# Kernel tuning notes

Measured on AMD Instinct MI355X. Metric: run time of the kernel, lower is better.

The kernel has to match this reference:

```python
import jax, jax.numpy as jnp
import numpy as np

C, H, W, NC, LC = 512, 160, 160, 1203, 64


def setup_inputs() -> dict:
    key = jax.random.key(0)
    ks = jax.random.split(key, 8)
    return {
        "cls_feat": jax.random.normal(ks[0], (1, C, H, W), jnp.float32),
        "loc_feat": jax.random.normal(ks[1], (1, LC, H, W), jnp.float32),
        "conf": jax.random.uniform(ks[2], (1,), jnp.float32, 0.2, 0.8),
        "pf_w": jax.random.normal(ks[3], (C,), jnp.float32) * 0.02,   # pf 1x1 conv, C->1
        "pf_b": jnp.zeros((1,), jnp.float32),
        "vocab_w": jax.random.normal(ks[4], (NC, C), jnp.float32) * 0.02,  # conv2linear weight
        "vocab_b": jnp.zeros((NC,), jnp.float32),
        "loc_w": jax.random.normal(ks[5], (LC, LC), jnp.float32) * 0.02,   # loc 1x1 conv
        "loc_b": jnp.zeros((LC,), jnp.float32),
    }


def reference(cls_feat, loc_feat, conf, pf_w, pf_b, vocab_w, vocab_b, loc_w, loc_b):
    B, Cc, Hh, Ww = cls_feat.shape
    # proposal-filter score: 1x1 conv C->1 on batch 0, flattened to [HW]
    pf_score = jnp.einsum('c,chw->hw', pf_w, cls_feat[0]).reshape(-1) + pf_b  # [HW]
    mask = jax.nn.sigmoid(pf_score) > conf[0]  # [HW] bool
    # tokens: [1, HW, C]
    tok = cls_feat.reshape(B, Cc, Hh * Ww).transpose(0, 2, 1)
    # static-shape equivalent of the proposal filter: zero masked-out tokens
    tok = tok * mask[None, :, None].astype(tok.dtype)
    # vocab linear (converted 1x1 conv): [1, HW, NC] -> [1, NC, HW]
    cls_out = (jnp.einsum('bnc,vc->bnv', tok, vocab_w) + vocab_b).transpose(0, 2, 1)
    # localization 1x1 conv
    loc_out = jnp.einsum('oi,bihw->bohw', loc_w, loc_feat) + loc_b[None, :, None, None]
    return loc_out, cls_out, mask
```

## Files before the change

### kernel.cpp

```cpp
#include <hip/hip_runtime.h>
#include <math.h>


constexpr int C_    = 512;
constexpr int HW_   = 25600;
constexpr int NC_   = 1203;
constexpr int VPAD_ = 1216;

constexpr int LOC_OFF_  = 0;
constexpr int CLS_OFF_  = 64 * HW_;
constexpr int MASK_OFF_ = CLS_OFF_ + NC_ * HW_;

constexpr int PF_BLOCKS_    = HW_ / 64;
constexpr int TRANS_BLOCKS_ = 19 * 8;
constexpr int GEMM_BLOCKS_  = 19 * 256;
constexpr int LOC_BLOCKS_   = 400;
constexpr int FILL_BLOCKS_  = 2048;

typedef float vfloat4 __attribute__((ext_vector_type(4)));

__global__ void k_init(int* cnt) { *cnt = 0; }

__global__ __launch_bounds__(256) void k_pre(
    const float* __restrict__ cls_feat, const float* __restrict__ conf,
    const float* __restrict__ pf_w, const float* __restrict__ pf_b,
    const float* __restrict__ vocab_w, float* __restrict__ out,
    int* __restrict__ cnt, int* __restrict__ idxList,
    float* __restrict__ AT4, int jcap)
{
    const int bid = blockIdx.x;
    const int tid = threadIdx.x;

    if (bid < PF_BLOCKS_) {
        __shared__ double sPart[256];
        const int hwi   = tid & 63;
        const int slice = tid >> 6;
        const int hw    = bid * 64 + hwi;
        const float* p  = cls_feat + (size_t)slice * 128 * HW_ + hw;
        const float* w  = pf_w + slice * 128;
        double acc = 0.0;
        #pragma unroll 4
        for (int k = 0; k < 128; ++k)
            acc += (double)w[k] * (double)p[(size_t)k * HW_];
        sPart[tid] = acc;
        __syncthreads();
        if (slice == 0) {
            double s = sPart[hwi] + sPart[64 + hwi] + sPart[128 + hwi] +
                       sPart[192 + hwi] + (double)pf_b[0];
            double sig = 1.0 / (1.0 + exp(-s));
            bool m = sig > (double)conf[0];
            out[MASK_OFF_ + hw] = m ? 1.0f : 0.0f;
            if (m) {
                int pos = atomicAdd(cnt, 1);
                if (pos < HW_) idxList[pos] = hw;
            }
        }
    } else {
        if (jcap <= 0) return;
        const int tb = bid - PF_BLOCKS_;
        const int v0 = (tb % 19) * 64;
        const int k0 = (tb / 19) * 64;
        __shared__ float t[64][65];
        const int c  = tid & 63;
        const int r4 = tid >> 6;
        #pragma unroll
        for (int i = 0; i < 16; ++i) {
            const int r = r4 * 16 + i;
            const int v = v0 + r;
            t[r][c] = (v < NC_) ? vocab_w[(size_t)v * C_ + k0 + c] : 0.f;
        }
        __syncthreads();
        #pragma unroll
        for (int i = 0; i < 16; ++i) {
            const int k  = r4 * 16 + i;
            const int kg = k0 + k;
            AT4[((size_t)(kg >> 2) * VPAD_ + v0 + c) * 4 + (kg & 3)] = t[c][k];
        }
    }
}

__global__ __launch_bounds__(256) void k_gatherJ(
    const float* __restrict__ cls_feat, const int* __restrict__ cnt,
    const int* __restrict__ idxList, float* __restrict__ BdT, int jcap)
{
    const int count = min(*cnt, HW_);
    if (count > jcap) return;
    const int t = threadIdx.x;
    for (int j = blockIdx.x; j < count; j += gridDim.x) {
        const int hw = idxList[j];
        BdT[(size_t)j * C_ + t]       = cls_feat[(size_t)t * HW_ + hw];
        BdT[(size_t)j * C_ + 256 + t] = cls_feat[(size_t)(256 + t) * HW_ + hw];
    }
}

__global__ __launch_bounds__(256) void k_mega(
    const float* __restrict__ loc_feat, const float* __restrict__ vocab_b,
    const float* __restrict__ loc_w, const float* __restrict__ loc_b,
    const float* __restrict__ AT4, const int* __restrict__ cnt,
    const float* __restrict__ BdT, float* __restrict__ clsTmp,
    float* __restrict__ out, int jcap)
{
    const int bid = blockIdx.x;
    const int tid = threadIdx.x;

    if (bid < GEMM_BLOCKS_) {
        const int count = min(*cnt, HW_);
        if (count == 0 || count > jcap) return;
        const int jBase = (bid / 19) * 4;
        if (jBase >= count) return;

        const int lane = tid & 63;
        const int w    = __builtin_amdgcn_readfirstlane(tid >> 6);
        const int v0   = (bid % 19) * 64;
        const int v    = v0 + lane;
        const float* __restrict__ Acol = AT4 + (size_t)v * 4;

        const int j0 = jBase + 0, j1 = jBase + 1, j2 = jBase + 2, j3 = jBase + 3;
        const float* __restrict__ B0 = BdT + (size_t)(j0 < count ? j0 : 0) * C_;
        const float* __restrict__ B1 = BdT + (size_t)(j1 < count ? j1 : 0) * C_;
        const float* __restrict__ B2 = BdT + (size_t)(j2 < count ? j2 : 0) * C_;
        const float* __restrict__ B3 = BdT + (size_t)(j3 < count ? j3 : 0) * C_;

        vfloat4 ac0 = {0,0,0,0}, ac1 = {0,0,0,0}, ac2 = {0,0,0,0}, ac3 = {0,0,0,0};
        const int kqBeg = w * 32;
        #pragma unroll 8
        for (int q = 0; q < 32; ++q) {
            const int kq = kqBeg + q;
            const vfloat4 a  = *(const vfloat4*)(Acol + (size_t)kq * VPAD_ * 4);
            const vfloat4 b0 = *(const vfloat4*)(B0 + kq * 4);
            const vfloat4 b1 = *(const vfloat4*)(B1 + kq * 4);
            const vfloat4 b2 = *(const vfloat4*)(B2 + kq * 4);
            const vfloat4 b3 = *(const vfloat4*)(B3 + kq * 4);
            ac0 += a * b0; ac1 += a * b1; ac2 += a * b2; ac3 += a * b3;
        }

        __shared__ float sRed[4][4][64];
        sRed[w][0][lane] = (ac0.x + ac0.y) + (ac0.z + ac0.w);
        sRed[w][1][lane] = (ac1.x + ac1.y) + (ac1.z + ac1.w);
        sRed[w][2][lane] = (ac2.x + ac2.y) + (ac2.z + ac2.w);
        sRed[w][3][lane] = (ac3.x + ac3.y) + (ac3.z + ac3.w);
        __syncthreads();

        if (tid < 64) {
            const float bias = (v < NC_) ? vocab_b[v] : 0.f;
            #pragma unroll
            for (int jj = 0; jj < 4; ++jj) {
                const int j = jBase + jj;
                if (j < count) {
                    const float s =
                        (sRed[0][jj][lane] + sRed[1][jj][lane]) +
                        (sRed[2][jj][lane] + sRed[3][jj][lane]);
                    clsTmp[(size_t)j * VPAD_ + v] = s + bias;
                }
            }
        }
    } else if (bid < GEMM_BLOCKS_ + LOC_BLOCKS_) {
        const int j   = bid - GEMM_BLOCKS_;
        const int hwb = j % 100;
        const int o0  = (j / 100) * 16;
        __shared__ float sw[16][64];
        for (int i = tid; i < 16 * 64; i += 256)
            sw[i >> 6][i & 63] = loc_w[(o0 + (i >> 6)) * 64 + (i & 63)];
        __syncthreads();
        const int hw = hwb * 256 + tid;
        float acc[16];
        #pragma unroll
        for (int r = 0; r < 16; ++r) acc[r] = loc_b[o0 + r];
        for (int i = 0; i < 64; ++i) {
            float f = loc_feat[(size_t)i * HW_ + hw];
            #pragma unroll
            for (int r = 0; r < 16; ++r) acc[r] += sw[r][i] * f;
        }
        #pragma unroll
        for (int r = 0; r < 16; ++r)
            out[LOC_OFF_ + (size_t)(o0 + r) * HW_ + hw] = acc[r];
    } else {
        const int fb = bid - GEMM_BLOCKS_ - LOC_BLOCKS_;
        const int total4 = NC_ * HW_ / 4;
        vfloat4* o = (vfloat4*)(out + CLS_OFF_);
        for (int i = fb * 256 + tid; i < total4; i += FILL_BLOCKS_ * 256) {
            int v = i / (HW_ / 4);
            float b = vocab_b[v];
            vfloat4 val = {b, b, b, b};
            __builtin_nontemporal_store(val, &o[i]);
        }
    }
}

__global__ __launch_bounds__(256) void k_scatter(
    const int* __restrict__ cnt, const int* __restrict__ idxList,
    const float* __restrict__ clsTmp, float* __restrict__ out, int jcap)
{
    const int count = min(*cnt, HW_);
    if (count > jcap) return;
    const int j = blockIdx.x;
    if (j >= count) return;
    const int hw = idxList[j];
    const float* __restrict__ src = clsTmp + (size_t)j * VPAD_;
    for (int v = threadIdx.x; v < NC_; v += 256)
        out[CLS_OFF_ + (size_t)v * HW_ + hw] = src[v];
}

__global__ __launch_bounds__(256) void k_gemm_fallback(
    const float* __restrict__ cls_feat, const float* __restrict__ vocab_w,
    const float* __restrict__ vocab_b, const int* __restrict__ cnt,
    const int* __restrict__ idxList, float* __restrict__ out, int capB)
{
    const int count = min(*cnt, HW_);
    if (count <= capB) return;
    const int v0 = blockIdx.x * 64;

    __shared__ float sAT[16][64];
    __shared__ float sBT[16][64];
    __shared__ int   sIdx[64];

    const int tid = threadIdx.x;
    const int tx = tid & 15;
    const int ty = tid >> 4;
    const int r  = tid >> 2;
    const int kq = tid & 3;

    for (int jb = blockIdx.y; (jb << 6) < count; jb += gridDim.y) {
        const int j0 = jb << 6;
        __syncthreads();
        if (tid < 64) {
            int j = j0 + tid;
            sIdx[tid] = (j < count) ? idxList[j] : -1;
        }
        __syncthreads();
        const int hwj = sIdx[r];

        float acc[4][4] = {};
        for (int k0 = 0; k0 < C_; k0 += 16) {
            float4 a4 = make_float4(0.f, 0.f, 0.f, 0.f);
            if (v0 + r < NC_)
                a4 = *(const float4*)(vocab_w + (size_t)(v0 + r) * C_ + k0 + kq * 4);
            float b0 = 0.f, b1 = 0.f, b2 = 0.f, b3 = 0.f;
            if (hwj >= 0) {
                const float* bp = cls_feat + (size_t)(k0 + kq * 4) * HW_ + hwj;
                b0 = bp[0]; b1 = bp[HW_]; b2 = bp[2 * HW_]; b3 = bp[3 * HW_];
            }
            __syncthreads();
            sAT[kq * 4 + 0][r] = a4.x; sAT[kq * 4 + 1][r] = a4.y;
            sAT[kq * 4 + 2][r] = a4.z; sAT[kq * 4 + 3][r] = a4.w;
            sBT[kq * 4 + 0][r] = b0;   sBT[kq * 4 + 1][r] = b1;
            sBT[kq * 4 + 2][r] = b2;   sBT[kq * 4 + 3][r] = b3;
            __syncthreads();
            #pragma unroll
            for (int kk = 0; kk < 16; ++kk) {
                const float4 av = *(const float4*)&sAT[kk][ty * 4];
                const float4 bv = *(const float4*)&sBT[kk][tx * 4];
                acc[0][0] += av.x * bv.x; acc[0][1] += av.x * bv.y;
                acc[0][2] += av.x * bv.z; acc[0][3] += av.x * bv.w;
                acc[1][0] += av.y * bv.x; acc[1][1] += av.y * bv.y;
                acc[1][2] += av.y * bv.z; acc[1][3] += av.y * bv.w;
                acc[2][0] += av.z * bv.x; acc[2][1] += av.z * bv.y;
                acc[2][2] += av.z * bv.z; acc[2][3] += av.z * bv.w;
                acc[3][0] += av.w * bv.x; acc[3][1] += av.w * bv.y;
                acc[3][2] += av.w * bv.z; acc[3][3] += av.w * bv.w;
            }
        }
        #pragma unroll
        for (int a = 0; a < 4; ++a) {
            int v = v0 + ty * 4 + a;
            if (v >= NC_) continue;
            float bias = vocab_b[v];
            #pragma unroll
            for (int b = 0; b < 4; ++b) {
                int j = j0 + tx * 4 + b;
                if (j < count) {
                    int hw = sIdx[tx * 4 + b];
                    out[CLS_OFF_ + (size_t)v * HW_ + hw] = acc[a][b] + bias;
                }
            }
        }
    }
}

extern "C" void kernel_launch(void* const* d_in, const int* in_sizes, int n_in,
                              void* d_out, int out_size, void* d_ws,
                              size_t ws_size, hipStream_t stream) {
    const float* cls_feat = (const float*)d_in[0];
    const float* loc_feat = (const float*)d_in[1];
    const float* conf     = (const float*)d_in[2];
    const float* pf_w     = (const float*)d_in[3];
    const float* pf_b     = (const float*)d_in[4];
    const float* vocab_w  = (const float*)d_in[5];
    const float* vocab_b  = (const float*)d_in[6];
    const float* loc_w    = (const float*)d_in[7];
    const float* loc_b    = (const float*)d_in[8];
    float* out = (float*)d_out;

    int*   cnt      = (int*)d_ws;
    int*   idxList  = (int*)((char*)d_ws + 4096);
    size_t fixed    = 4096 + (size_t)HW_ * sizeof(int);
    size_t atBytes  = (size_t)(C_ / 4) * VPAD_ * 4 * sizeof(float);
    size_t bdtBytes = (size_t)1024 * C_ * sizeof(float);
    size_t tmpBytes = (size_t)1024 * VPAD_ * sizeof(float);
    float* AT4      = (float*)((char*)d_ws + fixed);
    float* BdT      = (float*)((char*)d_ws + fixed + atBytes);
    float* clsTmp   = (float*)((char*)d_ws + fixed + atBytes + bdtBytes);

    int jcap = 0;
    if (ws_size >= fixed + atBytes + bdtBytes + tmpBytes) jcap = 1024;

    hipLaunchKernelGGL(k_init, dim3(1), dim3(1), 0, stream, cnt);
    hipLaunchKernelGGL(k_pre, dim3(PF_BLOCKS_ + TRANS_BLOCKS_), dim3(256),
                       0, stream,
                       cls_feat, conf, pf_w, pf_b, vocab_w, out, cnt,
                       idxList, AT4, jcap);
    if (jcap > 0) {
        hipLaunchKernelGGL(k_gatherJ, dim3(512), dim3(256), 0, stream,
                           cls_feat, cnt, idxList, BdT, jcap);
    }
    hipLaunchKernelGGL(k_mega,
                       dim3(GEMM_BLOCKS_ + LOC_BLOCKS_ + FILL_BLOCKS_),
                       dim3(256), 0, stream,
                       loc_feat, vocab_b, loc_w, loc_b, AT4, cnt, BdT,
                       clsTmp, out, jcap);
    if (jcap > 0) {
        hipLaunchKernelGGL(k_scatter, dim3(1024), dim3(256), 0, stream,
                           cnt, idxList, clsTmp, out, jcap);
    }
    hipLaunchKernelGGL(k_gemm_fallback, dim3((NC_ + 63) / 64, 8), dim3(256),
                       0, stream, cls_feat, vocab_w, vocab_b, cnt, idxList,
                       out, jcap);
}
```

Before: 68.71 us.

## Fuse cls scatter into bias fill via per-pixel row lookup table

The pre-pass now writes, for each pixel, its compacted row index, or -1 when the pixel is masked out. The bias-fill loop reads this table and writes GEMM results from clsTmp straight into the output, so the separate scatter kernel and its strided writes go away. The sparse GEMM moves out of the mega kernel into its own launch so its results are ready before the fill runs. This adds one launch, one lookup-table read per output vector and gathered reads from clsTmp, and the GEMM no longer overlaps with the loc/fill work.

```diff
diff --git a/kernel.cpp b/kernel.cpp
--- a/kernel.cpp
+++ b/kernel.cpp
@@ -13,7 +13,6 @@
 
 constexpr int PF_BLOCKS_    = HW_ / 64;
 constexpr int TRANS_BLOCKS_ = 19 * 8;
-constexpr int GEMM_BLOCKS_  = 19 * 256;
 constexpr int LOC_BLOCKS_   = 400;
 constexpr int FILL_BLOCKS_  = 2048;
 
@@ -26,7 +25,7 @@
     const float* __restrict__ pf_w, const float* __restrict__ pf_b,
     const float* __restrict__ vocab_w, float* __restrict__ out,
     int* __restrict__ cnt, int* __restrict__ idxList,
-    float* __restrict__ AT4, int jcap)
+    int* __restrict__ jLut, float* __restrict__ AT4, int jcap)
 {
     const int bid = blockIdx.x;
     const int tid = threadIdx.x;
@@ -50,10 +49,12 @@
             double sig = 1.0 / (1.0 + exp(-s));
             bool m = sig > (double)conf[0];
             out[MASK_OFF_ + hw] = m ? 1.0f : 0.0f;
+            int pos = -1;
             if (m) {
-                int pos = atomicAdd(cnt, 1);
+                pos = atomicAdd(cnt, 1);
                 if (pos < HW_) idxList[pos] = hw;
             }
+            jLut[hw] = (m && pos >= 0 && pos < jcap) ? pos : -1;
         }
     } else {
         if (jcap <= 0) return;
@@ -93,69 +94,75 @@
     }
 }
 
+__global__ __launch_bounds__(256) void k_gemm6t(
+    const float* __restrict__ AT4, const float* __restrict__ vocab_b,
+    const int* __restrict__ cnt, const float* __restrict__ BdT,
+    float* __restrict__ clsTmp, int jcap)
+{
+    const int count = min(*cnt, HW_);
+    if (count == 0 || count > jcap) return;
+    const int jBase = blockIdx.y * 4;
+    if (jBase >= count) return;
+
+    const int tid  = threadIdx.x;
+    const int lane = tid & 63;
+    const int w    = __builtin_amdgcn_readfirstlane(tid >> 6);
+    const int v0   = blockIdx.x * 64;
+    const int v    = v0 + lane;
+    const float* __restrict__ Acol = AT4 + (size_t)v * 4;
+
+    const int j0 = jBase + 0, j1 = jBase + 1, j2 = jBase + 2, j3 = jBase + 3;
+    const float* __restrict__ B0 = BdT + (size_t)(j0 < count ? j0 : 0) * C_;
+    const float* __restrict__ B1 = BdT + (size_t)(j1 < count ? j1 : 0) * C_;
+    const float* __restrict__ B2 = BdT + (size_t)(j2 < count ? j2 : 0) * C_;
+    const float* __restrict__ B3 = BdT + (size_t)(j3 < count ? j3 : 0) * C_;
+
+    vfloat4 ac0 = {0,0,0,0}, ac1 = {0,0,0,0}, ac2 = {0,0,0,0}, ac3 = {0,0,0,0};
+    const int kqBeg = w * 32;
+    #pragma unroll 8
+    for (int q = 0; q < 32; ++q) {
+        const int kq = kqBeg + q;
+        const vfloat4 a  = *(const vfloat4*)(Acol + (size_t)kq * VPAD_ * 4);
+        const vfloat4 b0 = *(const vfloat4*)(B0 + kq * 4);
+        const vfloat4 b1 = *(const vfloat4*)(B1 + kq * 4);
+        const vfloat4 b2 = *(const vfloat4*)(B2 + kq * 4);
+        const vfloat4 b3 = *(const vfloat4*)(B3 + kq * 4);
+        ac0 += a * b0; ac1 += a * b1; ac2 += a * b2; ac3 += a * b3;
+    }
+
+    __shared__ float sRed[4][4][64];
+    sRed[w][0][lane] = (ac0.x + ac0.y) + (ac0.z + ac0.w);
+    sRed[w][1][lane] = (ac1.x + ac1.y) + (ac1.z + ac1.w);
+    sRed[w][2][lane] = (ac2.x + ac2.y) + (ac2.z + ac2.w);
+    sRed[w][3][lane] = (ac3.x + ac3.y) + (ac3.z + ac3.w);
+    __syncthreads();
+
+    if (tid < 64) {
+        const float bias = (v < NC_) ? vocab_b[v] : 0.f;
+        #pragma unroll
+        for (int jj = 0; jj < 4; ++jj) {
+            const int j = jBase + jj;
+            if (j < count) {
+                const float s =
+                    (sRed[0][jj][lane] + sRed[1][jj][lane]) +
+                    (sRed[2][jj][lane] + sRed[3][jj][lane]);
+                clsTmp[(size_t)j * VPAD_ + v] = s + bias;
+            }
+        }
+    }
+}
+
 __global__ __launch_bounds__(256) void k_mega(
     const float* __restrict__ loc_feat, const float* __restrict__ vocab_b,
     const float* __restrict__ loc_w, const float* __restrict__ loc_b,
-    const float* __restrict__ AT4, const int* __restrict__ cnt,
-    const float* __restrict__ BdT, float* __restrict__ clsTmp,
-    float* __restrict__ out, int jcap)
+    const int* __restrict__ cnt, const int* __restrict__ jLut,
+    const float* __restrict__ clsTmp, float* __restrict__ out, int jcap)
 {
     const int bid = blockIdx.x;
     const int tid = threadIdx.x;
 
-    if (bid < GEMM_BLOCKS_) {
-        const int count = min(*cnt, HW_);
-        if (count == 0 || count > jcap) return;
-        const int jBase = (bid / 19) * 4;
-        if (jBase >= count) return;
-
-        const int lane = tid & 63;
-        const int w    = __builtin_amdgcn_readfirstlane(tid >> 6);
-        const int v0   = (bid % 19) * 64;
-        const int v    = v0 + lane;
-        const float* __restrict__ Acol = AT4 + (size_t)v * 4;
-
-        const int j0 = jBase + 0, j1 = jBase + 1, j2 = jBase + 2, j3 = jBase + 3;
-        const float* __restrict__ B0 = BdT + (size_t)(j0 < count ? j0 : 0) * C_;
-        const float* __restrict__ B1 = BdT + (size_t)(j1 < count ? j1 : 0) * C_;
-        const float* __restrict__ B2 = BdT + (size_t)(j2 < count ? j2 : 0) * C_;
-        const float* __restrict__ B3 = BdT + (size_t)(j3 < count ? j3 : 0) * C_;
-
-        vfloat4 ac0 = {0,0,0,0}, ac1 = {0,0,0,0}, ac2 = {0,0,0,0}, ac3 = {0,0,0,0};
-        const int kqBeg = w * 32;
-        #pragma unroll 8
-        for (int q = 0; q < 32; ++q) {
-            const int kq = kqBeg + q;
-            const vfloat4 a  = *(const vfloat4*)(Acol + (size_t)kq * VPAD_ * 4);
-            const vfloat4 b0 = *(const vfloat4*)(B0 + kq * 4);
-            const vfloat4 b1 = *(const vfloat4*)(B1 + kq * 4);
-            const vfloat4 b2 = *(const vfloat4*)(B2 + kq * 4);
-            const vfloat4 b3 = *(const vfloat4*)(B3 + kq * 4);
-            ac0 += a * b0; ac1 += a * b1; ac2 += a * b2; ac3 += a * b3;
-        }
-
-        __shared__ float sRed[4][4][64];
-        sRed[w][0][lane] = (ac0.x + ac0.y) + (ac0.z + ac0.w);
-        sRed[w][1][lane] = (ac1.x + ac1.y) + (ac1.z + ac1.w);
-        sRed[w][2][lane] = (ac2.x + ac2.y) + (ac2.z + ac2.w);
-        sRed[w][3][lane] = (ac3.x + ac3.y) + (ac3.z + ac3.w);
-        __syncthreads();
-
-        if (tid < 64) {
-            const float bias = (v < NC_) ? vocab_b[v] : 0.f;
-            #pragma unroll
-            for (int jj = 0; jj < 4; ++jj) {
-                const int j = jBase + jj;
-                if (j < count) {
-                    const float s =
-                        (sRed[0][jj][lane] + sRed[1][jj][lane]) +
-                        (sRed[2][jj][lane] + sRed[3][jj][lane]);
-                    clsTmp[(size_t)j * VPAD_ + v] = s + bias;
-                }
-            }
-        }
-    } else if (bid < GEMM_BLOCKS_ + LOC_BLOCKS_) {
-        const int j   = bid - GEMM_BLOCKS_;
+    if (bid < LOC_BLOCKS_) {
+        const int j   = bid;
         const int hwb = j % 100;
         const int o0  = (j / 100) * 16;
         __shared__ float sw[16][64];
@@ -175,30 +182,31 @@
         for (int r = 0; r < 16; ++r)
             out[LOC_OFF_ + (size_t)(o0 + r) * HW_ + hw] = acc[r];
     } else {
-        const int fb = bid - GEMM_BLOCKS_ - LOC_BLOCKS_;
+        const int fb     = bid - LOC_BLOCKS_;
+        const int count  = min(*cnt, HW_);
+        const bool live  = (jcap > 0) && (count > 0) && (count <= jcap);
+        const int hw4    = HW_ / 4;
         const int total4 = NC_ * HW_ / 4;
+        const int4* jLut4 = (const int4*)jLut;
         vfloat4* o = (vfloat4*)(out + CLS_OFF_);
         for (int i = fb * 256 + tid; i < total4; i += FILL_BLOCKS_ * 256) {
-            int v = i / (HW_ / 4);
-            float b = vocab_b[v];
+            const int v   = i / hw4;
+            const int rem = i - v * hw4;
+            const float b = vocab_b[v];
             vfloat4 val = {b, b, b, b};
+            if (live) {
+                const int4 jl = jLut4[rem];
+                if ((jl.x | jl.y | jl.z | jl.w) >= 0 ||
+                    jl.x >= 0 || jl.y >= 0 || jl.z >= 0 || jl.w >= 0) {
+                    if (jl.x >= 0) val.x = clsTmp[(size_t)jl.x * VPAD_ + v];
+                    if (jl.y >= 0) val.y = clsTmp[(size_t)jl.y * VPAD_ + v];
+                    if (jl.z >= 0) val.z = clsTmp[(size_t)jl.z * VPAD_ + v];
+                    if (jl.w >= 0) val.w = clsTmp[(size_t)jl.w * VPAD_ + v];
+                }
+            }
             __builtin_nontemporal_store(val, &o[i]);
         }
     }
-}
-
-__global__ __launch_bounds__(256) void k_scatter(
-    const int* __restrict__ cnt, const int* __restrict__ idxList,
-    const float* __restrict__ clsTmp, float* __restrict__ out, int jcap)
-{
-    const int count = min(*cnt, HW_);
-    if (count > jcap) return;
-    const int j = blockIdx.x;
-    if (j >= count) return;
-    const int hw = idxList[j];
-    const float* __restrict__ src = clsTmp + (size_t)j * VPAD_;
-    for (int v = threadIdx.x; v < NC_; v += 256)
-        out[CLS_OFF_ + (size_t)v * HW_ + hw] = src[v];
 }
 
 __global__ __launch_bounds__(256) void k_gemm_fallback(
@@ -293,7 +301,8 @@
 
     int*   cnt      = (int*)d_ws;
     int*   idxList  = (int*)((char*)d_ws + 4096);
-    size_t fixed    = 4096 + (size_t)HW_ * sizeof(int);
+    int*   jLut     = (int*)((char*)d_ws + 4096 + (size_t)HW_ * 4);
+    size_t fixed    = 4096 + (size_t)HW_ * 4 * 2;
     size_t atBytes  = (size_t)(C_ / 4) * VPAD_ * 4 * sizeof(float);
     size_t bdtBytes = (size_t)1024 * C_ * sizeof(float);
     size_t tmpBytes = (size_t)1024 * VPAD_ * sizeof(float);
@@ -308,20 +317,17 @@
     hipLaunchKernelGGL(k_pre, dim3(PF_BLOCKS_ + TRANS_BLOCKS_), dim3(256),
                        0, stream,
                        cls_feat, conf, pf_w, pf_b, vocab_w, out, cnt,
-                       idxList, AT4, jcap);
+                       idxList, jLut, AT4, jcap);
     if (jcap > 0) {
         hipLaunchKernelGGL(k_gatherJ, dim3(512), dim3(256), 0, stream,
                            cls_feat, cnt, idxList, BdT, jcap);
-    }
-    hipLaunchKernelGGL(k_mega,
-                       dim3(GEMM_BLOCKS_ + LOC_BLOCKS_ + FILL_BLOCKS_),
-                       dim3(256), 0, stream,
-                       loc_feat, vocab_b, loc_w, loc_b, AT4, cnt, BdT,
-                       clsTmp, out, jcap);
-    if (jcap > 0) {
-        hipLaunchKernelGGL(k_scatter, dim3(1024), dim3(256), 0, stream,
-                           cnt, idxList, clsTmp, out, jcap);
-    }
+        hipLaunchKernelGGL(k_gemm6t, dim3(19, 1024 / 4), dim3(256), 0, stream,
+                           AT4, vocab_b, cnt, BdT, clsTmp, jcap);
+    }
+    hipLaunchKernelGGL(k_mega, dim3(LOC_BLOCKS_ + FILL_BLOCKS_), dim3(256),
+                       0, stream,
+                       loc_feat, vocab_b, loc_w, loc_b, cnt, jLut, clsTmp,
+                       out, jcap);
     hipLaunchKernelGGL(k_gemm_fallback, dim3((NC_ + 63) / 64, 8), dim3(256),
                        0, stream, cls_feat, vocab_w, vocab_b, cnt, idxList,
                        out, jcap);
```

Measured after the change: 70.23 us. 1.02x slower.
